# Optimization experiments

Hardware: AMD Instinct MI355X
Metric: run time of the kernel (lower is better)

The kernel has to match this reference:

```python
import jax, jax.numpy as jnp
import numpy as np

N_NODES = 100000
N_EDGES = 1600000
N_GRAPHS = 256
K_HOPS = 3


def setup_inputs() -> dict:
    key = jax.random.key(0)
    ks = jax.random.split(key, 10)
    x = jax.random.normal(ks[0], (N_NODES, 32), dtype=jnp.float32)
    edge_index = jax.random.randint(ks[1], (2, N_EDGES), 0, N_NODES, dtype=jnp.int32)
    batch = jnp.sort(jax.random.randint(ks[2], (N_NODES,), 0, N_GRAPHS, dtype=jnp.int32))
    gcn_w = jax.random.normal(ks[3], (64, 32), dtype=jnp.float32) * 0.1
    gcn_b = jax.random.normal(ks[4], (64,), dtype=jnp.float32) * 0.1
    w1 = jax.random.normal(ks[5], (32, 64), dtype=jnp.float32) * 0.1
    b1 = jax.random.normal(ks[6], (32,), dtype=jnp.float32) * 0.1
    w2 = jax.random.normal(ks[7], (16, 32), dtype=jnp.float32) * 0.1
    b2 = jax.random.normal(ks[8], (16,), dtype=jnp.float32) * 0.1
    return {"x": x, "edge_index": edge_index, "batch": batch,
            "gcn_w": gcn_w, "gcn_b": gcn_b, "w1": w1, "b1": b1, "w2": w2, "b2": b2}


def reference(x, edge_index, batch, gcn_w, gcn_b, w1, b1, w2, b2):
    N = x.shape[0]
    src, dst = edge_index[0], edge_index[1]
    # GCN symmetric normalization with self-loops: deg = in-degree + 1
    deg = jax.ops.segment_sum(jnp.ones_like(src, dtype=x.dtype), dst, num_segments=N) + 1.0
    norm = deg ** -0.5  # [N]
    h = x
    for _ in range(K_HOPS):
        # edge message: norm[src] * h[src], scattered to dst, scaled by norm[dst];
        # self-loop contributes norm[i]^2 * h[i]
        msg = h[src] * norm[src][:, None]                     # [E, C]
        agg = jax.ops.segment_sum(msg, dst, num_segments=N)    # [N, C]
        h = norm[:, None] * agg + (norm * norm)[:, None] * h
    h = jax.nn.relu(h @ gcn_w.T + gcn_b)                       # [N, hidden]
    # global mean pool per graph
    counts = jax.ops.segment_sum(jnp.ones((N,), x.dtype), batch, num_segments=N_GRAPHS)
    sums = jax.ops.segment_sum(h, batch, num_segments=N_GRAPHS)
    h_avg = sums / jnp.maximum(counts, 1.0)[:, None]           # [G, hidden]
    # classifier (dropout = identity in eval)
    h1 = jax.nn.relu(h_avg @ w1.T + b1)
    logits = h1 @ w2.T + b2                                    # [G, nc]
    return logits
```

## Files before the change

### kernel.cpp

```cpp
#include <hip/hip_runtime.h>

constexpr int NW    = 391;
constexpr int CH    = 6400;
constexpr int CAP_B = 8192;
constexpr int CAP_C = 10240;

__device__ __forceinline__ unsigned bf16_rne(float x) {
    unsigned u = __float_as_uint(x);
    u += 0x7fffu + ((u >> 16) & 1u);
    return u >> 16;
}
__device__ __forceinline__ unsigned pack2(float even, float odd) {
    return bf16_rne(even) | (bf16_rne(odd) << 16);
}
__device__ __forceinline__ float lo_f(unsigned u) { return __uint_as_float(u << 16); }
__device__ __forceinline__ float hi_f(unsigned u) { return __uint_as_float(u & 0xffff0000u); }


__global__ __launch_bounds__(512) void k_bucket(const int* __restrict__ src,
                                                const int* __restrict__ dst, int E,
                                                int* __restrict__ wcur, int* __restrict__ packed) {
    __shared__ int h[256];
    __shared__ int base[256];
    int t = threadIdx.x;
    if (t < 256) h[t] = 0;
    __syncthreads();
    int b0 = blockIdx.x * CH;
    int cnt = min(CH, E - b0);
    if (cnt == CH) {
        const int4* d4 = (const int4*)(dst + b0);
        for (int i = t; i < CH / 4; i += 512) {
            int4 v = d4[i];
            atomicAdd(&h[v.x / NW], 1); atomicAdd(&h[v.y / NW], 1);
            atomicAdd(&h[v.z / NW], 1); atomicAdd(&h[v.w / NW], 1);
        }
    } else {
        for (int i = t; i < cnt; i += 512) atomicAdd(&h[dst[b0 + i] / NW], 1);
    }
    __syncthreads();
    if (t < 256) { base[t] = atomicAdd(&wcur[t], h[t]); h[t] = 0; }
    __syncthreads();
    if (cnt == CH) {
        const int4* d4 = (const int4*)(dst + b0);
        const int4* s4 = (const int4*)(src + b0);
        for (int i = t; i < CH / 4; i += 512) {
            int4 dv = d4[i];
            int4 sv = s4[i];
            int da[4] = {dv.x, dv.y, dv.z, dv.w};
            int sa[4] = {sv.x, sv.y, sv.z, sv.w};
#pragma unroll
            for (int j = 0; j < 4; ++j) {
                int w = da[j] / NW;
                int l = da[j] - w * NW;
                int r = atomicAdd(&h[w], 1);
                int pos = base[w] + r;
                if (pos < CAP_B) packed[w * CAP_B + pos] = (l << 17) | sa[j];
            }
        }
    } else {
        for (int i = t; i < cnt; i += 512) {
            int d = dst[b0 + i];
            int s = src[b0 + i];
            int w = d / NW;
            int l = d - w * NW;
            int r = atomicAdd(&h[w], 1);
            int pos = base[w] + r;
            if (pos < CAP_B) packed[w * CAP_B + pos] = (l << 17) | s;
        }
    }
}


__global__ __launch_bounds__(512) void k_window(const int* __restrict__ packed,
                                                const int* __restrict__ wcur,
                                                const float4* __restrict__ x4,
                                                float* __restrict__ norm,
                                                int2* __restrict__ rng,
                                                int* __restrict__ csr,
                                                uint2* __restrict__ hb, int N, int W) {
    __shared__ int hist[NW];
    __shared__ float snorm[NW];
    __shared__ int pend[NW];
    __shared__ int cur[NW];
    __shared__ int wpart[8];
    int t = threadIdx.x, w = blockIdx.x;
    int lo = w * NW, nwn = min(NW, N - lo);
    for (int i = t; i < NW; i += 512) hist[i] = 0;
    __syncthreads();
    int cnt = min(wcur[w], CAP_B);
    const int* pk = packed + (size_t)w * CAP_B;
    for (int e = t; e < cnt; e += 512) atomicAdd(&hist[pk[e] >> 17], 1);
    __syncthreads();
    int d = (t < nwn) ? hist[t] : 0;
    float nv = rsqrtf((float)(d + 1));
    if (t < nwn) { snorm[t] = nv; norm[lo + t] = nv; }
    int pd = (t < nwn) ? ((d + 7) & ~7) : 0;
    int lane = t & 63, wid = t >> 6;
    int v = pd;
#pragma unroll
    for (int s = 1; s < 64; s <<= 1) {
        int u = __shfl_up(v, s, 64);
        if (lane >= s) v += u;
    }
    if (lane == 63) wpart[wid] = v;
    __syncthreads();
    if (t < 8) {
        int z = wpart[t];
#pragma unroll
        for (int s = 1; s < 8; s <<= 1) {
            int u = __shfl_up(z, s, 8);
            if (t >= s) z += u;
        }
        wpart[t] = z;
    }
    __syncthreads();
    int incl = v + (wid ? wpart[wid - 1] : 0);
    int base = w * CAP_C;
    int cend = base + incl;
    if (t < nwn) {
        rng[lo + t] = make_int2(cend - pd, cend);
        pend[t] = cend;
        cur[t] = cend - pd;
    }
    if (w == W - 1 && t == 0) { norm[N] = 1.f; rng[N] = make_int2(0, 0); }
    __syncthreads();
    for (int e = t; e < cnt; e += 512) {
        int p = pk[e];
        int pos = atomicAdd(&cur[p >> 17], 1);
        csr[pos] = p & 0x1FFFF;
    }
    __syncthreads();
    if (t < nwn) {
        for (int pos = cur[t]; pos < pend[t]; ++pos) csr[pos] = N;
    }
    for (int idx = t; idx < nwn * 8; idx += 512) {
        int node = idx >> 3, q = idx & 7;
        float nn = snorm[node];
        float4 vx = x4[(size_t)(lo + node) * 8 + q];
        hb[(size_t)(lo + node) * 8 + q] =
            make_uint2(pack2(vx.x * nn, vx.y * nn), pack2(vx.z * nn, vx.w * nn));
    }
    if (w == W - 1 && t < 8) hb[(size_t)N * 8 + t] = make_uint2(0u, 0u);
}

__global__ __launch_bounds__(256) void k_hop(const uint4* __restrict__ tab,
                                             const float* __restrict__ norm,
                                             const int2* __restrict__ rng,
                                             const int* __restrict__ csr,
                                             uint4* __restrict__ outb, int N) {
    int group = (blockIdx.x * blockDim.x + threadIdx.x) >> 2;
    int l = threadIdx.x & 3;
    if (group > N) return;
    uint4 sv = tab[(size_t)group * 4 + l];
    float a0 = lo_f(sv.x), a1 = hi_f(sv.x), a2 = lo_f(sv.y), a3 = hi_f(sv.y);
    float a4 = lo_f(sv.z), a5 = hi_f(sv.z), a6 = lo_f(sv.w), a7 = hi_f(sv.w);
    int2 be = rng[group];
    for (int k = be.x; k < be.y; k += 8) {
        int e0 = csr[k + l];
        int e1 = csr[k + 4 + l];
        uint4 u[8];
#pragma unroll
        for (int j = 0; j < 4; ++j) {
            int s = __shfl(e0, j, 4);
            u[j] = tab[(size_t)s * 4 + l];
        }
#pragma unroll
        for (int j = 0; j < 4; ++j) {
            int s = __shfl(e1, j, 4);
            u[4 + j] = tab[(size_t)s * 4 + l];
        }
#pragma unroll
        for (int j = 0; j < 8; ++j) {
            a0 += lo_f(u[j].x); a1 += hi_f(u[j].x);
            a2 += lo_f(u[j].y); a3 += hi_f(u[j].y);
            a4 += lo_f(u[j].z); a5 += hi_f(u[j].z);
            a6 += lo_f(u[j].w); a7 += hi_f(u[j].w);
        }
    }
    float n = norm[group];
    float sc = n * n;
    outb[(size_t)group * 4 + l] = make_uint4(pack2(a0 * sc, a1 * sc), pack2(a2 * sc, a3 * sc),
                                             pack2(a4 * sc, a5 * sc), pack2(a6 * sc, a7 * sc));
}

__global__ __launch_bounds__(256) void k_hopfeat(const uint4* __restrict__ tab,
                                                 const float* __restrict__ norm,
                                                 const int2* __restrict__ rng,
                                                 const int* __restrict__ csr,
                                                 const int* __restrict__ batch,
                                                 const float* __restrict__ gw,
                                                 const float* __restrict__ gb,
                                                 float* __restrict__ gsum, int N) {
    __shared__ __align__(16) float wT[32][64];
    __shared__ float bs[64];
    __shared__ float accw[4][64];
    int t = threadIdx.x;
    int wid = t >> 6;
    {
        int c = t & 63;
#pragma unroll
        for (int iter = 0; iter < 8; ++iter) {
            int k = iter * 4 + wid;
            wT[k][c] = gw[c * 32 + k];
        }
    }
    if (t < 64) bs[t] = gb[t];
    __syncthreads();
    int group = (blockIdx.x * 256 + t) >> 2;
    int l = t & 3;
    float a[8] = {0.f, 0.f, 0.f, 0.f, 0.f, 0.f, 0.f, 0.f};
    if (group <= N) {
        uint4 sv = tab[(size_t)group * 4 + l];
        a[0] = lo_f(sv.x); a[1] = hi_f(sv.x); a[2] = lo_f(sv.y); a[3] = hi_f(sv.y);
        a[4] = lo_f(sv.z); a[5] = hi_f(sv.z); a[6] = lo_f(sv.w); a[7] = hi_f(sv.w);
        int2 be = rng[group];
        for (int k = be.x; k < be.y; k += 8) {
            int e0 = csr[k + l];
            int e1 = csr[k + 4 + l];
            uint4 u[8];
#pragma unroll
            for (int j = 0; j < 4; ++j) {
                int s = __shfl(e0, j, 4);
                u[j] = tab[(size_t)s * 4 + l];
            }
#pragma unroll
            for (int j = 0; j < 4; ++j) {
                int s = __shfl(e1, j, 4);
                u[4 + j] = tab[(size_t)s * 4 + l];
            }
#pragma unroll
            for (int j = 0; j < 8; ++j) {
                a[0] += lo_f(u[j].x); a[1] += hi_f(u[j].x);
                a[2] += lo_f(u[j].y); a[3] += hi_f(u[j].y);
                a[4] += lo_f(u[j].z); a[5] += hi_f(u[j].z);
                a[6] += lo_f(u[j].w); a[7] += hi_f(u[j].w);
            }
        }
        float n = norm[group];
#pragma unroll
        for (int j = 0; j < 8; ++j) a[j] *= n;
    }
    float o[16];
#pragma unroll
    for (int cc = 0; cc < 16; ++cc) o[cc] = 0.f;
    int gmy = 0x7fffffff;
    if (group < N) {
        gmy = batch[group];
        float d[16];
#pragma unroll
        for (int cc = 0; cc < 16; ++cc) d[cc] = bs[l * 16 + cc];
#pragma unroll
        for (int k = 0; k < 32; ++k) {
            float hk = __shfl(a[k & 7], k >> 3, 4);
            const float4* wv = (const float4*)&wT[k][l * 16];
            float4 w0 = wv[0], w1 = wv[1], w2 = wv[2], w3 = wv[3];
            d[0]  += hk * w0.x; d[1]  += hk * w0.y; d[2]  += hk * w0.z; d[3]  += hk * w0.w;
            d[4]  += hk * w1.x; d[5]  += hk * w1.y; d[6]  += hk * w1.z; d[7]  += hk * w1.w;
            d[8]  += hk * w2.x; d[9]  += hk * w2.y; d[10] += hk * w2.z; d[11] += hk * w2.w;
            d[12] += hk * w3.x; d[13] += hk * w3.y; d[14] += hk * w3.z; d[15] += hk * w3.w;
        }
#pragma unroll
        for (int cc = 0; cc < 16; ++cc) o[cc] = fmaxf(d[cc], 0.f);
    }
    int n0 = blockIdx.x * 64;
    int g0 = batch[min(n0, N - 1)];
    int g1 = batch[min(n0 + 63, N - 1)];
    bool leader = (t & 0x3C) == 0;
    for (int g = g0; g <= g1; ++g) {
        float v[16];
#pragma unroll
        for (int cc = 0; cc < 16; ++cc) {
            float val = (gmy == g) ? o[cc] : 0.f;
            val += __shfl_xor(val, 4, 64);
            val += __shfl_xor(val, 8, 64);
            val += __shfl_xor(val, 16, 64);
            val += __shfl_xor(val, 32, 64);
            v[cc] = val;
        }
        if (leader) {
#pragma unroll
            for (int cc = 0; cc < 16; ++cc) accw[wid][l * 16 + cc] = v[cc];
        }
        __syncthreads();
        if (t < 64) {
            float s = accw[0][t] + accw[1][t] + accw[2][t] + accw[3][t];
            if (s != 0.f) atomicAdd(&gsum[(size_t)g * 64 + t], s);
        }
        __syncthreads();
    }
}


__global__ __launch_bounds__(64) void k_head(const float* __restrict__ gsum,
                                             const int* __restrict__ batch, int N,
                                             const float* __restrict__ w1, const float* __restrict__ b1,
                                             const float* __restrict__ w2, const float* __restrict__ b2,
                                             float* __restrict__ out) {
    __shared__ float havg[64];
    __shared__ float h1s[32];
    __shared__ int se[2];
    int t = threadIdx.x, g = blockIdx.x;
    if (t < 2) {
        int target = g + t;
        int lo = 0, hi = N;
        while (lo < hi) { int mid = (lo + hi) >> 1; if (batch[mid] < target) lo = mid + 1; else hi = mid; }
        se[t] = lo;
    }
    __syncthreads();
    int cnt = se[1] - se[0];
    float inv = 1.f / (float)(cnt > 0 ? cnt : 1);
    havg[t] = gsum[(size_t)g * 64 + t] * inv;
    __syncthreads();
    if (t < 32) {
        float d = b1[t];
#pragma unroll
        for (int k = 0; k < 64; ++k) d += havg[k] * w1[t * 64 + k];
        h1s[t] = fmaxf(d, 0.f);
    }
    __syncthreads();
    if (t < 16) {
        float d = b2[t];
#pragma unroll
        for (int j = 0; j < 32; ++j) d += h1s[j] * w2[t * 32 + j];
        out[g * 16 + t] = d;
    }
}


extern "C" void kernel_launch(void* const* d_in, const int* in_sizes, int n_in,
                              void* d_out, int out_size, void* d_ws, size_t ws_size,
                              hipStream_t stream) {
    const float* x     = (const float*)d_in[0];
    const int*   ei    = (const int*)d_in[1];
    const int*   batch = (const int*)d_in[2];
    const float* gw    = (const float*)d_in[3];
    const float* gb    = (const float*)d_in[4];
    const float* w1    = (const float*)d_in[5];
    const float* b1    = (const float*)d_in[6];
    const float* w2    = (const float*)d_in[7];
    const float* b2    = (const float*)d_in[8];
    float* out = (float*)d_out;

    int N = in_sizes[2];
    int E = in_sizes[1] / 2;
    int G = out_size / 16;
    const int* srcp = ei;
    const int* dstp = ei + E;

    int W  = (N + NW - 1) / NW;
    int NB = (E + CH - 1) / CH;

    char* ws = (char*)d_ws;
    size_t off = 0;
    auto alloc = [&](size_t bytes) -> void* {
        void* p = ws + off;
        off += (bytes + 255) & ~(size_t)255;
        return p;
    };
    int*   wcur   = (int*)alloc(256 * 4 + (size_t)G * 64 * 4);
    float* gsum   = (float*)(wcur + 256);
    int*   packed = (int*)alloc((size_t)W * CAP_B * 4);
    int*   csr    = (int*)alloc((size_t)W * CAP_C * 4);
    int2*  rng    = (int2*)alloc((size_t)(N + 1) * 8);
    float* norm   = (float*)alloc((size_t)(N + 1) * 4);
    uint2* hbA    = (uint2*)alloc((size_t)(N + 1) * 64);
    uint2* hbB    = (uint2*)alloc((size_t)(N + 1) * 64);

    hipMemsetAsync(wcur, 0, 256 * 4 + (size_t)G * 64 * 4, stream);

    int pb4 = ((N + 1) * 4 + 255) / 256;

    k_bucket<<<NB, 512, 0, stream>>>(srcp, dstp, E, wcur, packed);
    k_window<<<W, 512, 0, stream>>>(packed, wcur, (const float4*)x, norm, rng, csr, hbA, N, W);

    k_hop<<<pb4, 256, 0, stream>>>((const uint4*)hbA, norm, rng, csr, (uint4*)hbB, N);
    k_hop<<<pb4, 256, 0, stream>>>((const uint4*)hbB, norm, rng, csr, (uint4*)hbA, N);
    k_hopfeat<<<pb4, 256, 0, stream>>>((const uint4*)hbA, norm, rng, csr, batch, gw, gb, gsum, N);

    k_head<<<G, 64, 0, stream>>>(gsum, batch, N, w1, b1, w2, b2, out);
}
```

Baseline: 197.0 us.

## Split feature table into channel halves and run hops per half

Stores the bf16 feature table as two separate 16-channel halves (32 bytes per node each), so each hop pass gathers from a 3.2 MB table instead of a 6.4 MB one, which is meant to fit better in cache and raise the hit rate for random neighbour gathers. Each hop now runs as two half-kernels, using two lanes per node and nontemporal CSR loads. The last hop writes fp32 features into a buffer that reuses the packed bucket space, and a separate k_feat kernel does the linear layer and pooling. This doubles the number of CSR scans and kernel launches, and adds an fp32 round trip for the final features.

```diff
diff --git a/kernel.cpp b/kernel.cpp
--- a/kernel.cpp
+++ b/kernel.cpp
@@ -77,7 +77,7 @@
                                                 float* __restrict__ norm,
                                                 int2* __restrict__ rng,
                                                 int* __restrict__ csr,
-                                                uint2* __restrict__ hb, int N, int W) {
+                                                uint4* __restrict__ hb, int N, int W) {
     __shared__ int hist[NW];
     __shared__ float snorm[NW];
     __shared__ int pend[NW];
@@ -85,6 +85,7 @@
     __shared__ int wpart[8];
     int t = threadIdx.x, w = blockIdx.x;
     int lo = w * NW, nwn = min(NW, N - lo);
+    size_t HALF = (size_t)(N + 1) * 2;
     for (int i = t; i < NW; i += 512) hist[i] = 0;
     __syncthreads();
     int cnt = min(wcur[w], CAP_B);
@@ -133,42 +134,49 @@
     if (t < nwn) {
         for (int pos = cur[t]; pos < pend[t]; ++pos) csr[pos] = N;
     }
-    for (int idx = t; idx < nwn * 8; idx += 512) {
-        int node = idx >> 3, q = idx & 7;
+    for (int idx = t; idx < nwn * 4; idx += 512) {
+        int node = idx >> 2, r = idx & 3;
         float nn = snorm[node];
-        float4 vx = x4[(size_t)(lo + node) * 8 + q];
-        hb[(size_t)(lo + node) * 8 + q] =
-            make_uint2(pack2(vx.x * nn, vx.y * nn), pack2(vx.z * nn, vx.w * nn));
-    }
-    if (w == W - 1 && t < 8) hb[(size_t)N * 8 + t] = make_uint2(0u, 0u);
-}
-
-__global__ __launch_bounds__(256) void k_hop(const uint4* __restrict__ tab,
-                                             const float* __restrict__ norm,
-                                             const int2* __restrict__ rng,
-                                             const int* __restrict__ csr,
-                                             uint4* __restrict__ outb, int N) {
-    int group = (blockIdx.x * blockDim.x + threadIdx.x) >> 2;
-    int l = threadIdx.x & 3;
+        float4 va = x4[(size_t)(lo + node) * 8 + r * 2];
+        float4 vb = x4[(size_t)(lo + node) * 8 + r * 2 + 1];
+        hb[(size_t)(r >> 1) * HALF + (size_t)(lo + node) * 2 + (r & 1)] =
+            make_uint4(pack2(va.x * nn, va.y * nn), pack2(va.z * nn, va.w * nn),
+                       pack2(vb.x * nn, vb.y * nn), pack2(vb.z * nn, vb.w * nn));
+    }
+    if (w == W - 1 && t < 4)
+        hb[(size_t)(t >> 1) * HALF + (size_t)N * 2 + (t & 1)] = make_uint4(0u, 0u, 0u, 0u);
+}
+
+template <int MODE>
+__global__ __launch_bounds__(256) void k_hop_half(const uint4* __restrict__ tab,
+                                                  const float* __restrict__ norm,
+                                                  const int2* __restrict__ rng,
+                                                  const int* __restrict__ csr,
+                                                  uint4* __restrict__ outb,
+                                                  float4* __restrict__ outf,
+                                                  int half, int N) {
+    int gid = blockIdx.x * 256 + threadIdx.x;
+    int group = gid >> 1;
+    int l = gid & 1;
     if (group > N) return;
-    uint4 sv = tab[(size_t)group * 4 + l];
+    uint4 sv = tab[(size_t)group * 2 + l];
     float a0 = lo_f(sv.x), a1 = hi_f(sv.x), a2 = lo_f(sv.y), a3 = hi_f(sv.y);
     float a4 = lo_f(sv.z), a5 = hi_f(sv.z), a6 = lo_f(sv.w), a7 = hi_f(sv.w);
     int2 be = rng[group];
     for (int k = be.x; k < be.y; k += 8) {
-        int e0 = csr[k + l];
-        int e1 = csr[k + 4 + l];
+        int r0 = __builtin_nontemporal_load(csr + k + l);
+        int r1 = __builtin_nontemporal_load(csr + k + 2 + l);
+        int r2 = __builtin_nontemporal_load(csr + k + 4 + l);
+        int r3 = __builtin_nontemporal_load(csr + k + 6 + l);
         uint4 u[8];
 #pragma unroll
-        for (int j = 0; j < 4; ++j) {
-            int s = __shfl(e0, j, 4);
-            u[j] = tab[(size_t)s * 4 + l];
-        }
-#pragma unroll
-        for (int j = 0; j < 4; ++j) {
-            int s = __shfl(e1, j, 4);
-            u[4 + j] = tab[(size_t)s * 4 + l];
-        }
+        for (int j = 0; j < 2; ++j) u[j]     = tab[(size_t)__shfl(r0, j, 2) * 2 + l];
+#pragma unroll
+        for (int j = 0; j < 2; ++j) u[2 + j] = tab[(size_t)__shfl(r1, j, 2) * 2 + l];
+#pragma unroll
+        for (int j = 0; j < 2; ++j) u[4 + j] = tab[(size_t)__shfl(r2, j, 2) * 2 + l];
+#pragma unroll
+        for (int j = 0; j < 2; ++j) u[6 + j] = tab[(size_t)__shfl(r3, j, 2) * 2 + l];
 #pragma unroll
         for (int j = 0; j < 8; ++j) {
             a0 += lo_f(u[j].x); a1 += hi_f(u[j].x);
@@ -178,19 +186,23 @@
         }
     }
     float n = norm[group];
-    float sc = n * n;
-    outb[(size_t)group * 4 + l] = make_uint4(pack2(a0 * sc, a1 * sc), pack2(a2 * sc, a3 * sc),
-                                             pack2(a4 * sc, a5 * sc), pack2(a6 * sc, a7 * sc));
-}
-
-__global__ __launch_bounds__(256) void k_hopfeat(const uint4* __restrict__ tab,
-                                                 const float* __restrict__ norm,
-                                                 const int2* __restrict__ rng,
-                                                 const int* __restrict__ csr,
-                                                 const int* __restrict__ batch,
-                                                 const float* __restrict__ gw,
-                                                 const float* __restrict__ gb,
-                                                 float* __restrict__ gsum, int N) {
+    if (MODE == 0) {
+        float sc = n * n;
+        outb[(size_t)group * 2 + l] =
+            make_uint4(pack2(a0 * sc, a1 * sc), pack2(a2 * sc, a3 * sc),
+                       pack2(a4 * sc, a5 * sc), pack2(a6 * sc, a7 * sc));
+    } else {
+        size_t b = (size_t)group * 8 + half * 4 + l * 2;
+        outf[b]     = make_float4(a0 * n, a1 * n, a2 * n, a3 * n);
+        outf[b + 1] = make_float4(a4 * n, a5 * n, a6 * n, a7 * n);
+    }
+}
+
+__global__ __launch_bounds__(256) void k_feat(const float4* __restrict__ hF,
+                                              const int* __restrict__ batch,
+                                              const float* __restrict__ gw,
+                                              const float* __restrict__ gb,
+                                              float* __restrict__ gsum, int N) {
     __shared__ __align__(16) float wT[32][64];
     __shared__ float bs[64];
     __shared__ float accw[4][64];
@@ -208,43 +220,14 @@
     __syncthreads();
     int group = (blockIdx.x * 256 + t) >> 2;
     int l = t & 3;
-    float a[8] = {0.f, 0.f, 0.f, 0.f, 0.f, 0.f, 0.f, 0.f};
-    if (group <= N) {
-        uint4 sv = tab[(size_t)group * 4 + l];
-        a[0] = lo_f(sv.x); a[1] = hi_f(sv.x); a[2] = lo_f(sv.y); a[3] = hi_f(sv.y);
-        a[4] = lo_f(sv.z); a[5] = hi_f(sv.z); a[6] = lo_f(sv.w); a[7] = hi_f(sv.w);
-        int2 be = rng[group];
-        for (int k = be.x; k < be.y; k += 8) {
-            int e0 = csr[k + l];
-            int e1 = csr[k + 4 + l];
-            uint4 u[8];
-#pragma unroll
-            for (int j = 0; j < 4; ++j) {
-                int s = __shfl(e0, j, 4);
-                u[j] = tab[(size_t)s * 4 + l];
-            }
-#pragma unroll
-            for (int j = 0; j < 4; ++j) {
-                int s = __shfl(e1, j, 4);
-                u[4 + j] = tab[(size_t)s * 4 + l];
-            }
-#pragma unroll
-            for (int j = 0; j < 8; ++j) {
-                a[0] += lo_f(u[j].x); a[1] += hi_f(u[j].x);
-                a[2] += lo_f(u[j].y); a[3] += hi_f(u[j].y);
-                a[4] += lo_f(u[j].z); a[5] += hi_f(u[j].z);
-                a[6] += lo_f(u[j].w); a[7] += hi_f(u[j].w);
-            }
-        }
-        float n = norm[group];
-#pragma unroll
-        for (int j = 0; j < 8; ++j) a[j] *= n;
-    }
     float o[16];
 #pragma unroll
     for (int cc = 0; cc < 16; ++cc) o[cc] = 0.f;
     int gmy = 0x7fffffff;
     if (group < N) {
+        float4 v0 = hF[(size_t)group * 8 + l * 2];
+        float4 v1 = hF[(size_t)group * 8 + l * 2 + 1];
+        float a[8] = {v0.x, v0.y, v0.z, v0.w, v1.x, v1.y, v1.z, v1.w};
         gmy = batch[group];
         float d[16];
 #pragma unroll
@@ -359,23 +342,36 @@
     };
     int*   wcur   = (int*)alloc(256 * 4 + (size_t)G * 64 * 4);
     float* gsum   = (float*)(wcur + 256);
-    int*   packed = (int*)alloc((size_t)W * CAP_B * 4);
+    size_t unionBytes = (size_t)W * CAP_B * 4;
+    size_t hfBytes = (size_t)(N + 1) * 128;
+    if (hfBytes > unionBytes) unionBytes = hfBytes;
+    int*    packed = (int*)alloc(unionBytes);
+    float4* hF     = (float4*)packed;
     int*   csr    = (int*)alloc((size_t)W * CAP_C * 4);
     int2*  rng    = (int2*)alloc((size_t)(N + 1) * 8);
     float* norm   = (float*)alloc((size_t)(N + 1) * 4);
-    uint2* hbA    = (uint2*)alloc((size_t)(N + 1) * 64);
-    uint2* hbB    = (uint2*)alloc((size_t)(N + 1) * 64);
+    uint4* hbA    = (uint4*)alloc((size_t)(N + 1) * 64);
+    uint4* hbB    = (uint4*)alloc((size_t)(N + 1) * 64);
+
+    size_t HALF = (size_t)(N + 1) * 2;
+    uint4* A0 = hbA;           uint4* A1 = hbA + HALF;
+    uint4* B0 = hbB;           uint4* B1 = hbB + HALF;
 
     hipMemsetAsync(wcur, 0, 256 * 4 + (size_t)G * 64 * 4, stream);
 
+    int pb2 = ((N + 1) * 2 + 255) / 256;
     int pb4 = ((N + 1) * 4 + 255) / 256;
 
     k_bucket<<<NB, 512, 0, stream>>>(srcp, dstp, E, wcur, packed);
     k_window<<<W, 512, 0, stream>>>(packed, wcur, (const float4*)x, norm, rng, csr, hbA, N, W);
 
-    k_hop<<<pb4, 256, 0, stream>>>((const uint4*)hbA, norm, rng, csr, (uint4*)hbB, N);
-    k_hop<<<pb4, 256, 0, stream>>>((const uint4*)hbB, norm, rng, csr, (uint4*)hbA, N);
-    k_hopfeat<<<pb4, 256, 0, stream>>>((const uint4*)hbA, norm, rng, csr, batch, gw, gb, gsum, N);
-
+    k_hop_half<0><<<pb2, 256, 0, stream>>>(A0, norm, rng, csr, B0, nullptr, 0, N);
+    k_hop_half<0><<<pb2, 256, 0, stream>>>(A1, norm, rng, csr, B1, nullptr, 1, N);
+    k_hop_half<0><<<pb2, 256, 0, stream>>>(B0, norm, rng, csr, A0, nullptr, 0, N);
+    k_hop_half<0><<<pb2, 256, 0, stream>>>(B1, norm, rng, csr, A1, nullptr, 1, N);
+    k_hop_half<1><<<pb2, 256, 0, stream>>>(A0, norm, rng, csr, nullptr, hF, 0, N);
+    k_hop_half<1><<<pb2, 256, 0, stream>>>(A1, norm, rng, csr, nullptr, hF, 1, N);
+
+    k_feat<<<pb4, 256, 0, stream>>>(hF, batch, gw, gb, gsum, N);
     k_head<<<G, 64, 0, stream>>>(gsum, batch, N, w1, b1, w2, b2, out);
 }
```

After: 276.1 us. 1.4x slower.

## Stage CSR in LDS, unroll gather loop to 16 edges, fold gsum zeroing

Applied to the files above, without the earlier changes.

k_window now builds each window's CSR slice in shared memory and writes it out to global memory with coalesced int4 stores, instead of scattering atomically placed indices straight to global memory. It also writes the bf16 feature table with 16-byte stores, and it zeroes gsum in place of the larger memset. The hop kernels unroll the neighbor gather to 16 edges per iteration with a tail of 8, load CSR indices with nontemporal loads, and drop the launch_bounds annotation. The larger unroll raises the number of gathers in flight but also register pressure, and the 40KB LDS array limits k_window occupancy.

```diff
diff --git a/kernel.cpp b/kernel.cpp
--- a/kernel.cpp
+++ b/kernel.cpp
@@ -77,14 +77,22 @@
                                                 float* __restrict__ norm,
                                                 int2* __restrict__ rng,
                                                 int* __restrict__ csr,
-                                                uint2* __restrict__ hb, int N, int W) {
+                                                uint4* __restrict__ hb,
+                                                float* __restrict__ gsum,
+                                                int N, int W, int G) {
     __shared__ int hist[NW];
     __shared__ float snorm[NW];
     __shared__ int pend[NW];
     __shared__ int cur[NW];
     __shared__ int wpart[8];
+    __shared__ int stot;
+    __shared__ __align__(16) int lcsr[CAP_C];
     int t = threadIdx.x, w = blockIdx.x;
     int lo = w * NW, nwn = min(NW, N - lo);
+    {
+        int i = w * 512 + t;
+        if (i < G * 64) gsum[i] = 0.f;
+    }
     for (int i = t; i < NW; i += 512) hist[i] = 0;
     __syncthreads();
     int cnt = min(wcur[w], CAP_B);
@@ -115,39 +123,46 @@
     }
     __syncthreads();
     int incl = v + (wid ? wpart[wid - 1] : 0);
-    int base = w * CAP_C;
-    int cend = base + incl;
+    int gbase = w * CAP_C;
     if (t < nwn) {
-        rng[lo + t] = make_int2(cend - pd, cend);
-        pend[t] = cend;
-        cur[t] = cend - pd;
-    }
+        rng[lo + t] = make_int2(gbase + incl - pd, gbase + incl);
+        pend[t] = incl;
+        cur[t] = incl - pd;
+    }
+    if (t == 511) stot = incl;
     if (w == W - 1 && t == 0) { norm[N] = 1.f; rng[N] = make_int2(0, 0); }
     __syncthreads();
     for (int e = t; e < cnt; e += 512) {
         int p = pk[e];
         int pos = atomicAdd(&cur[p >> 17], 1);
-        csr[pos] = p & 0x1FFFF;
+        lcsr[pos] = p & 0x1FFFF;
     }
     __syncthreads();
     if (t < nwn) {
-        for (int pos = cur[t]; pos < pend[t]; ++pos) csr[pos] = N;
-    }
-    for (int idx = t; idx < nwn * 8; idx += 512) {
-        int node = idx >> 3, q = idx & 7;
+        for (int pos = cur[t]; pos < pend[t]; ++pos) lcsr[pos] = N;
+    }
+    __syncthreads();
+    {
+        int tot4 = stot >> 2;
+        int4* g4 = (int4*)(csr + gbase);
+        const int4* l4 = (const int4*)lcsr;
+        for (int i = t; i < tot4; i += 512) g4[i] = l4[i];
+    }
+    for (int idx = t; idx < nwn * 4; idx += 512) {
+        int node = idx >> 2, q = idx & 3;
         float nn = snorm[node];
-        float4 vx = x4[(size_t)(lo + node) * 8 + q];
-        hb[(size_t)(lo + node) * 8 + q] =
-            make_uint2(pack2(vx.x * nn, vx.y * nn), pack2(vx.z * nn, vx.w * nn));
-    }
-    if (w == W - 1 && t < 8) hb[(size_t)N * 8 + t] = make_uint2(0u, 0u);
-}
-
-__global__ __launch_bounds__(256) void k_hop(const uint4* __restrict__ tab,
-                                             const float* __restrict__ norm,
-                                             const int2* __restrict__ rng,
-                                             const int* __restrict__ csr,
-                                             uint4* __restrict__ outb, int N) {
+        float4 va = x4[(size_t)(lo + node) * 8 + q * 2];
+        float4 vb = x4[(size_t)(lo + node) * 8 + q * 2 + 1];
+        hb[(size_t)(lo + node) * 4 + q] =
+            make_uint4(pack2(va.x * nn, va.y * nn), pack2(va.z * nn, va.w * nn),
+                       pack2(vb.x * nn, vb.y * nn), pack2(vb.z * nn, vb.w * nn));
+    }
+    if (w == W - 1 && t < 4) hb[(size_t)N * 4 + t] = make_uint4(0u, 0u, 0u, 0u);
+}
+
+__global__ void k_hop(const uint4* __restrict__ tab, const float* __restrict__ norm,
+                      const int2* __restrict__ rng, const int* __restrict__ csr,
+                      uint4* __restrict__ outb, int N) {
     int group = (blockIdx.x * blockDim.x + threadIdx.x) >> 2;
     int l = threadIdx.x & 3;
     if (group > N) return;
@@ -155,20 +170,37 @@
     float a0 = lo_f(sv.x), a1 = hi_f(sv.x), a2 = lo_f(sv.y), a3 = hi_f(sv.y);
     float a4 = lo_f(sv.z), a5 = hi_f(sv.z), a6 = lo_f(sv.w), a7 = hi_f(sv.w);
     int2 be = rng[group];
-    for (int k = be.x; k < be.y; k += 8) {
-        int e0 = csr[k + l];
-        int e1 = csr[k + 4 + l];
+    int k = be.x;
+    for (; k + 16 <= be.y; k += 16) {
+        int e0 = __builtin_nontemporal_load(csr + k + l);
+        int e1 = __builtin_nontemporal_load(csr + k + 4 + l);
+        int e2 = __builtin_nontemporal_load(csr + k + 8 + l);
+        int e3 = __builtin_nontemporal_load(csr + k + 12 + l);
+        uint4 u[16];
+#pragma unroll
+        for (int j = 0; j < 4; ++j) u[j]      = tab[(size_t)__shfl(e0, j, 4) * 4 + l];
+#pragma unroll
+        for (int j = 0; j < 4; ++j) u[4 + j]  = tab[(size_t)__shfl(e1, j, 4) * 4 + l];
+#pragma unroll
+        for (int j = 0; j < 4; ++j) u[8 + j]  = tab[(size_t)__shfl(e2, j, 4) * 4 + l];
+#pragma unroll
+        for (int j = 0; j < 4; ++j) u[12 + j] = tab[(size_t)__shfl(e3, j, 4) * 4 + l];
+#pragma unroll
+        for (int j = 0; j < 16; ++j) {
+            a0 += lo_f(u[j].x); a1 += hi_f(u[j].x);
+            a2 += lo_f(u[j].y); a3 += hi_f(u[j].y);
+            a4 += lo_f(u[j].z); a5 += hi_f(u[j].z);
+            a6 += lo_f(u[j].w); a7 += hi_f(u[j].w);
+        }
+    }
+    if (k < be.y) {
+        int e0 = __builtin_nontemporal_load(csr + k + l);
+        int e1 = __builtin_nontemporal_load(csr + k + 4 + l);
         uint4 u[8];
 #pragma unroll
-        for (int j = 0; j < 4; ++j) {
-            int s = __shfl(e0, j, 4);
-            u[j] = tab[(size_t)s * 4 + l];
-        }
-#pragma unroll
-        for (int j = 0; j < 4; ++j) {
-            int s = __shfl(e1, j, 4);
-            u[4 + j] = tab[(size_t)s * 4 + l];
-        }
+        for (int j = 0; j < 4; ++j) u[j]     = tab[(size_t)__shfl(e0, j, 4) * 4 + l];
+#pragma unroll
+        for (int j = 0; j < 4; ++j) u[4 + j] = tab[(size_t)__shfl(e1, j, 4) * 4 + l];
 #pragma unroll
         for (int j = 0; j < 8; ++j) {
             a0 += lo_f(u[j].x); a1 += hi_f(u[j].x);
@@ -214,20 +246,37 @@
         a[0] = lo_f(sv.x); a[1] = hi_f(sv.x); a[2] = lo_f(sv.y); a[3] = hi_f(sv.y);
         a[4] = lo_f(sv.z); a[5] = hi_f(sv.z); a[6] = lo_f(sv.w); a[7] = hi_f(sv.w);
         int2 be = rng[group];
-        for (int k = be.x; k < be.y; k += 8) {
-            int e0 = csr[k + l];
-            int e1 = csr[k + 4 + l];
+        int k = be.x;
+        for (; k + 16 <= be.y; k += 16) {
+            int e0 = __builtin_nontemporal_load(csr + k + l);
+            int e1 = __builtin_nontemporal_load(csr + k + 4 + l);
+            int e2 = __builtin_nontemporal_load(csr + k + 8 + l);
+            int e3 = __builtin_nontemporal_load(csr + k + 12 + l);
+            uint4 u[16];
+#pragma unroll
+            for (int j = 0; j < 4; ++j) u[j]      = tab[(size_t)__shfl(e0, j, 4) * 4 + l];
+#pragma unroll
+            for (int j = 0; j < 4; ++j) u[4 + j]  = tab[(size_t)__shfl(e1, j, 4) * 4 + l];
+#pragma unroll
+            for (int j = 0; j < 4; ++j) u[8 + j]  = tab[(size_t)__shfl(e2, j, 4) * 4 + l];
+#pragma unroll
+            for (int j = 0; j < 4; ++j) u[12 + j] = tab[(size_t)__shfl(e3, j, 4) * 4 + l];
+#pragma unroll
+            for (int j = 0; j < 16; ++j) {
+                a[0] += lo_f(u[j].x); a[1] += hi_f(u[j].x);
+                a[2] += lo_f(u[j].y); a[3] += hi_f(u[j].y);
+                a[4] += lo_f(u[j].z); a[5] += hi_f(u[j].z);
+                a[6] += lo_f(u[j].w); a[7] += hi_f(u[j].w);
+            }
+        }
+        if (k < be.y) {
+            int e0 = __builtin_nontemporal_load(csr + k + l);
+            int e1 = __builtin_nontemporal_load(csr + k + 4 + l);
             uint4 u[8];
 #pragma unroll
-            for (int j = 0; j < 4; ++j) {
-                int s = __shfl(e0, j, 4);
-                u[j] = tab[(size_t)s * 4 + l];
-            }
-#pragma unroll
-            for (int j = 0; j < 4; ++j) {
-                int s = __shfl(e1, j, 4);
-                u[4 + j] = tab[(size_t)s * 4 + l];
-            }
+            for (int j = 0; j < 4; ++j) u[j]     = tab[(size_t)__shfl(e0, j, 4) * 4 + l];
+#pragma unroll
+            for (int j = 0; j < 4; ++j) u[4 + j] = tab[(size_t)__shfl(e1, j, 4) * 4 + l];
 #pragma unroll
             for (int j = 0; j < 8; ++j) {
                 a[0] += lo_f(u[j].x); a[1] += hi_f(u[j].x);
@@ -246,21 +295,21 @@
     int gmy = 0x7fffffff;
     if (group < N) {
         gmy = batch[group];
-        float d[16];
-#pragma unroll
-        for (int cc = 0; cc < 16; ++cc) d[cc] = bs[l * 16 + cc];
+        float dd[16];
+#pragma unroll
+        for (int cc = 0; cc < 16; ++cc) dd[cc] = bs[l * 16 + cc];
 #pragma unroll
         for (int k = 0; k < 32; ++k) {
             float hk = __shfl(a[k & 7], k >> 3, 4);
             const float4* wv = (const float4*)&wT[k][l * 16];
             float4 w0 = wv[0], w1 = wv[1], w2 = wv[2], w3 = wv[3];
-            d[0]  += hk * w0.x; d[1]  += hk * w0.y; d[2]  += hk * w0.z; d[3]  += hk * w0.w;
-            d[4]  += hk * w1.x; d[5]  += hk * w1.y; d[6]  += hk * w1.z; d[7]  += hk * w1.w;
-            d[8]  += hk * w2.x; d[9]  += hk * w2.y; d[10] += hk * w2.z; d[11] += hk * w2.w;
-            d[12] += hk * w3.x; d[13] += hk * w3.y; d[14] += hk * w3.z; d[15] += hk * w3.w;
-        }
-#pragma unroll
-        for (int cc = 0; cc < 16; ++cc) o[cc] = fmaxf(d[cc], 0.f);
+            dd[0]  += hk * w0.x; dd[1]  += hk * w0.y; dd[2]  += hk * w0.z; dd[3]  += hk * w0.w;
+            dd[4]  += hk * w1.x; dd[5]  += hk * w1.y; dd[6]  += hk * w1.z; dd[7]  += hk * w1.w;
+            dd[8]  += hk * w2.x; dd[9]  += hk * w2.y; dd[10] += hk * w2.z; dd[11] += hk * w2.w;
+            dd[12] += hk * w3.x; dd[13] += hk * w3.y; dd[14] += hk * w3.z; dd[15] += hk * w3.w;
+        }
+#pragma unroll
+        for (int cc = 0; cc < 16; ++cc) o[cc] = fmaxf(dd[cc], 0.f);
     }
     int n0 = blockIdx.x * 64;
     int g0 = batch[min(n0, N - 1)];
@@ -357,25 +406,26 @@
         off += (bytes + 255) & ~(size_t)255;
         return p;
     };
-    int*   wcur   = (int*)alloc(256 * 4 + (size_t)G * 64 * 4);
-    float* gsum   = (float*)(wcur + 256);
+    int*   wcur   = (int*)alloc(256 * 4);
+    float* gsum   = (float*)alloc((size_t)G * 64 * 4);
     int*   packed = (int*)alloc((size_t)W * CAP_B * 4);
     int*   csr    = (int*)alloc((size_t)W * CAP_C * 4);
     int2*  rng    = (int2*)alloc((size_t)(N + 1) * 8);
     float* norm   = (float*)alloc((size_t)(N + 1) * 4);
-    uint2* hbA    = (uint2*)alloc((size_t)(N + 1) * 64);
-    uint2* hbB    = (uint2*)alloc((size_t)(N + 1) * 64);
-
-    hipMemsetAsync(wcur, 0, 256 * 4 + (size_t)G * 64 * 4, stream);
+    uint4* hbA    = (uint4*)alloc((size_t)(N + 1) * 64);
+    uint4* hbB    = (uint4*)alloc((size_t)(N + 1) * 64);
+
+    hipMemsetAsync(wcur, 0, 256 * 4, stream);
 
     int pb4 = ((N + 1) * 4 + 255) / 256;
 
     k_bucket<<<NB, 512, 0, stream>>>(srcp, dstp, E, wcur, packed);
-    k_window<<<W, 512, 0, stream>>>(packed, wcur, (const float4*)x, norm, rng, csr, hbA, N, W);
-
-    k_hop<<<pb4, 256, 0, stream>>>((const uint4*)hbA, norm, rng, csr, (uint4*)hbB, N);
-    k_hop<<<pb4, 256, 0, stream>>>((const uint4*)hbB, norm, rng, csr, (uint4*)hbA, N);
-    k_hopfeat<<<pb4, 256, 0, stream>>>((const uint4*)hbA, norm, rng, csr, batch, gw, gb, gsum, N);
+    k_window<<<W, 512, 0, stream>>>(packed, wcur, (const float4*)x, norm, rng, csr,
+                                    hbA, gsum, N, W, G);
+
+    k_hop<<<pb4, 256, 0, stream>>>(hbA, norm, rng, csr, hbB, N);
+    k_hop<<<pb4, 256, 0, stream>>>(hbB, norm, rng, csr, hbA, N);
+    k_hopfeat<<<pb4, 256, 0, stream>>>(hbA, norm, rng, csr, batch, gw, gb, gsum, N);
 
     k_head<<<G, 64, 0, stream>>>(gsum, batch, N, w1, b1, w2, b2, out);
 }
```

Result: no change. 200.6 us (+1.8%).
